# Performance work log

Hardware: AMD Instinct MI355X
Metric: run time of the kernel (lower is better)

Reference implementation:

```python
import jax, jax.numpy as jnp
import numpy as np

K = 20
EPS_BN = 1e-5

def knn_idx(x, k):
    # x: [B,N,C] -> k nearest neighbor indices [B,N,k] (self included, as in DGCNN)
    sq = jnp.sum(x * x, axis=-1)                       # [B,N]
    inner = jnp.einsum('bnc,bmc->bnm', x, x)           # [B,N,N]
    neg_dist = 2.0 * inner - sq[:, :, None] - sq[:, None, :]
    _, idx = jax.lax.top_k(neg_dist, k)
    return jax.lax.stop_gradient(idx)

def edge_feat(x, idx):
    # x: [B,N,C], idx: [B,N,k] -> [B,N,k,2C] = cat([x_j - x_i, x_i])
    nbr = jax.vmap(lambda xb, ib: xb[ib])(x, idx)      # [B,N,k,C]
    ctr = jnp.broadcast_to(x[:, :, None, :], nbr.shape)
    return jnp.concatenate([nbr - ctr, ctr], axis=-1)

def edge_conv(x, W, g, b, k):
    e = edge_feat(x, knn_idx(x, k))                    # dynamic kNN graph per layer
    h = jnp.einsum('bnkc,cd->bnkd', e, W)              # 1x1 conv2d
    h = h * (g / jnp.sqrt(1.0 + EPS_BN)) + b           # BN eval (mean=0, var=1)
    return jnp.max(jax.nn.leaky_relu(h, 0.2), axis=2)  # max over neighbors -> [B,N,d]

def layer_norm(x, g, b):
    m = jnp.mean(x, axis=-1, keepdims=True)
    v = jnp.var(x, axis=-1, keepdims=True)
    return (x - m) * jax.lax.rsqrt(v + 1e-5) * g + b

def setup_inputs():
    key = jax.random.key(0)
    B, N = 2, 4096
    ks = jax.random.split(key, 16)
    w = lambda i, shape: jax.random.normal(ks[i], shape, jnp.float32) * 0.05
    ones = lambda d: jnp.ones((d,), jnp.float32)
    zeros = lambda d: jnp.zeros((d,), jnp.float32)
    return dict(
        xyz=jax.random.normal(ks[0], (N, 3), jnp.float32),
        scale=jax.random.normal(ks[1], (N, 3), jnp.float32),
        rot=jax.random.normal(ks[2], (N, 4), jnp.float32),
        opacity=jax.random.normal(ks[3], (N, 1), jnp.float32),
        color=jax.random.normal(ks[4], (N, 3), jnp.float32),
        pose=jax.random.normal(ks[5], (B, 75), jnp.float32),
        lbs_weights=jax.random.normal(ks[6], (N, 24), jnp.float32),
        Wc1=w(7, (226, 64)), g1=ones(64), b1=zeros(64),
        Wc2=w(8, (128, 64)), g2=ones(64), b2=zeros(64),
        Wc3=w(9, (128, 128)), g3=ones(128), b3=zeros(128),
        Wc4=w(10, (256, 256)), g4=ones(256), b4=zeros(256),
        Wc5=w(11, (512, 128)), g5=ones(128), b5=zeros(128),
        Wo1=w(12, (128, 128)), bo1=zeros(128), lg1=ones(128), lb1=zeros(128),
        Wo2=w(13, (128, 128)), bo2=zeros(128), lg2=ones(128), lb2=zeros(128),
        Wo3=w(14, (128, 38)), bo3=zeros(38),
    )

def reference(xyz, scale, rot, opacity, color, pose, lbs_weights,
              Wc1, g1, b1, Wc2, g2, b2, Wc3, g3, b3, Wc4, g4, b4, Wc5, g5, b5,
              Wo1, bo1, lg1, lb1, Wo2, bo2, lg2, lb2, Wo3, bo3):
    B, N = pose.shape[0], xyz.shape[0]
    gfeat = jnp.concatenate([xyz, scale, rot, opacity, color], axis=-1)   # [N,14]
    feats = jnp.concatenate([
        jnp.broadcast_to(gfeat[None], (B, N, gfeat.shape[-1])),
        jnp.broadcast_to(lbs_weights[None], (B, N, lbs_weights.shape[-1])),
        jnp.broadcast_to(pose[:, None, :], (B, N, pose.shape[-1])),
    ], axis=-1)                                                            # [B,N,113]
    # DGCNN graph encoder (dynamic kNN EdgeConv stack)
    x1 = edge_conv(feats, Wc1, g1, b1, K)   # [B,N,64]
    x2 = edge_conv(x1, Wc2, g2, b2, K)      # [B,N,64]
    x3 = edge_conv(x2, Wc3, g3, b3, K)      # [B,N,128]
    x4 = edge_conv(x3, Wc4, g4, b4, K)      # [B,N,256]
    cat = jnp.concatenate([x1, x2, x3, x4], axis=-1)                      # [B,N,512]
    gf = jax.nn.leaky_relu(
        jnp.einsum('bnc,cd->bnd', cat, Wc5) * (g5 / jnp.sqrt(1.0 + EPS_BN)) + b5, 0.2)
    # offset predictor MLP
    h = jax.nn.leaky_relu(layer_norm(gf @ Wo1 + bo1, lg1, lb1), 0.2)
    h = jax.nn.leaky_relu(layer_norm(h @ Wo2 + bo2, lg2, lb2), 0.2)
    off = h @ Wo3 + bo3                                                   # [B,N,38]
    # residual add of gaussian offsets (first 14 dims), lbs offsets raw (last 24)
    out = jnp.concatenate([gfeat[None] + off[..., :14], off[..., 14:]], axis=-1)
    return out                                                            # [B,N,38]
```

## Files before the change

### kernel.cpp

```cpp
#include <hip/hip_runtime.h>
#include <math.h>

#define KNN 20
#define BN_INV 0.9999950000374997f

__device__ __forceinline__ unsigned f2o(float f){
    unsigned u = __float_as_uint(f);
    return (u >> 31) ? ~u : (u | 0x80000000u);
}
__device__ __forceinline__ float o2f(unsigned u){
    return __uint_as_float((u >> 31) ? (u & 0x7fffffffu) : ~u);
}
__device__ __forceinline__ float leaky(float v){ return v > 0.f ? v : 0.2f * v; }

__global__ __launch_bounds__(128) void build_feats_kernel(
    const float* __restrict__ xyz, const float* __restrict__ scale,
    const float* __restrict__ rot, const float* __restrict__ opac,
    const float* __restrict__ color, const float* __restrict__ pose,
    const float* __restrict__ lbs, float* __restrict__ feats,
    float* __restrict__ sqout, int N)
{
    __shared__ float sred[2];
    int row = blockIdx.x;
    int b = row / N, n = row % N;
    int c = threadIdx.x;
    float v = 0.f;
    if      (c <   3) v = xyz  [n*3 + c];
    else if (c <   6) v = scale[n*3 + c-3];
    else if (c <  10) v = rot  [n*4 + c-6];
    else if (c <  11) v = opac [n];
    else if (c <  14) v = color[n*3 + c-11];
    else if (c <  38) v = lbs  [n*24 + c-14];
    else if (c < 113) v = pose [b*75 + c-38];
    if (c < 116) feats[(long)row*116 + c] = v;
    float ss = v * v;
    #pragma unroll
    for (int off = 32; off; off >>= 1) ss += __shfl_xor(ss, off);
    if ((c & 63) == 0) sred[c >> 6] = ss;
    __syncthreads();
    if (c == 0) sqout[row] = sred[0] + sred[1];
}


template<int C>
__global__ __launch_bounds__(256) void dist_gemm_kernel(
    const float* __restrict__ x, int N, int CP, float* __restrict__ G)
{
    __shared__ __align__(16) float smem[9216];
    float (*xi)[36] = (float(*)[36])smem;
    float (*xj)[36] = (float(*)[36])(smem + 128*36);

    const int q = blockIdx.x;
    int bjt = (int)((sqrtf(8.f*(float)q + 1.f) - 1.f) * 0.5f);
    while ((bjt+1)*(bjt+2)/2 <= q) ++bjt;
    while (bjt*(bjt+1)/2 > q) --bjt;
    const int bit = q - bjt*(bjt+1)/2;
    const int bi = bit * 128;
    const int bj = bjt * 128;

    const int b  = blockIdx.z;
    const int t  = threadIdx.x;
    const int tx = t & 15, ty = t >> 4;
    const int CP4 = CP / 4;
    const long base = (long)b * N;
    const float4* xp = (const float4*)x;

    float acc[8][8] = {};

    for (int c0 = 0; c0 < C; c0 += 32){
        const int KC  = (C - c0 < 32) ? (C - c0) : 32;
        const int KC4 = KC >> 2;
        __syncthreads();
        if (KC4 == 8){
            for (int f = t; f < 128 * 8; f += 256){
                int r = f >> 3, c4 = f & 7;
                *(float4*)&xi[r][c4 * 4] = xp[(base + bi + r) * CP4 + (c0 >> 2) + c4];
                *(float4*)&xj[r][c4 * 4] = xp[(base + bj + r) * CP4 + (c0 >> 2) + c4];
            }
        } else {
            for (int f = t; f < 128 * KC4; f += 256){
                int r = f / KC4, c4 = f - r * KC4;
                *(float4*)&xi[r][c4 * 4] = xp[(base + bi + r) * CP4 + (c0 >> 2) + c4];
                *(float4*)&xj[r][c4 * 4] = xp[(base + bj + r) * CP4 + (c0 >> 2) + c4];
            }
        }
        __syncthreads();
        for (int c = 0; c < KC; c += 4){
            float4 A[8], Bv[8];
            #pragma unroll
            for (int ii = 0; ii < 8; ++ii) A[ii]  = *(const float4*)&xi[ty + 16*ii][c];
            #pragma unroll
            for (int jj = 0; jj < 8; ++jj) Bv[jj] = *(const float4*)&xj[tx + 16*jj][c];
            #pragma unroll
            for (int ii = 0; ii < 8; ++ii)
                #pragma unroll
                for (int jj = 0; jj < 8; ++jj){
                    acc[ii][jj] = fmaf(A[ii].x, Bv[jj].x, acc[ii][jj]);
                    acc[ii][jj] = fmaf(A[ii].y, Bv[jj].y, acc[ii][jj]);
                    acc[ii][jj] = fmaf(A[ii].z, Bv[jj].z, acc[ii][jj]);
                    acc[ii][jj] = fmaf(A[ii].w, Bv[jj].w, acc[ii][jj]);
                }
        }
    }

    #pragma unroll
    for (int ii = 0; ii < 8; ++ii){
        long rbase = (base + bi + ty + 16*ii) * N + bj;
        #pragma unroll
        for (int jj = 0; jj < 8; ++jj)
            G[rbase + tx + 16*jj] = acc[ii][jj];
    }

    if (bi != bj){
        float (*tr)[132] = (float(*)[132])smem;
        #pragma unroll
        for (int h = 0; h < 2; ++h){
            __syncthreads();
            #pragma unroll
            for (int ii = 0; ii < 8; ++ii)
                #pragma unroll
                for (int jj = 4*h; jj < 4*h + 4; ++jj)
                    tr[tx + 16*(jj - 4*h)][ty + 16*ii] = acc[ii][jj];
            __syncthreads();
            const int cc = (t & 31) * 4;
            const int r0 = t >> 5;
            #pragma unroll
            for (int f = 0; f < 8; ++f){
                int r = r0 + 8 * f;
                *(float4*)&G[(base + bj + 64*h + r) * N + bi + cc] = *(const float4*)&tr[r][cc];
            }
        }
    }
}

#define TCAP 256
__global__ __launch_bounds__(256) void topk_kernel(
    const float* __restrict__ G, const float* __restrict__ sq,
    int N, int* __restrict__ idx_out)
{
    __shared__ unsigned smax[256];
    __shared__ unsigned cand_u[TCAP];
    __shared__ int      cand_j[TCAP];
    __shared__ unsigned cand_cnt;
    __shared__ unsigned sTu;

    const int row = blockIdx.x;
    const int b   = row >> 12;
    const int t   = threadIdx.x;
    const float4* g4  = (const float4*)(G  + (long)row * 4096);
    const float4* sq4 = (const float4*)(sq + (long)b   * 4096);

    unsigned u[16];
    #pragma unroll
    for (int qq = 0; qq < 4; ++qq){
        int v4 = t + 256 * qq;
        float4 gg = g4[v4];
        float4 ss = sq4[v4];
        u[4*qq+0] = f2o(fmaf(2.f, gg.x, -ss.x));
        u[4*qq+1] = f2o(fmaf(2.f, gg.y, -ss.y));
        u[4*qq+2] = f2o(fmaf(2.f, gg.z, -ss.z));
        u[4*qq+3] = f2o(fmaf(2.f, gg.w, -ss.w));
    }

    unsigned mu = u[0];
    #pragma unroll
    for (int q = 1; q < 16; ++q) mu = u[q] > mu ? u[q] : mu;
    smax[t] = mu;
    if (t == 0) cand_cnt = 0;
    __syncthreads();

    int rank = 0;
    for (int k = 0; k < 256; ++k){
        unsigned ou = smax[k];
        rank += (ou > mu) || (ou == mu && k < t);
    }
    if (rank == KNN - 1) sTu = mu;
    __syncthreads();
    const unsigned Tu = sTu;

    #pragma unroll
    for (int qq = 0; qq < 4; ++qq)
        #pragma unroll
        for (int m = 0; m < 4; ++m){
            int q = 4*qq + m;
            if (u[q] >= Tu){
                unsigned p = atomicAdd(&cand_cnt, 1u);
                if (p < TCAP){ cand_u[p] = u[q]; cand_j[p] = 4*(t + 256*qq) + m; }
            }
        }
    __syncthreads();
    const int cc = (int)cand_cnt;

    if (cc <= TCAP){
        if (t < cc){
            unsigned cu = cand_u[t]; int cj = cand_j[t];
            int r = 0;
            for (int k = 0; k < cc; ++k){
                unsigned ou = cand_u[k];
                r += (ou > cu) || (ou == cu && cand_j[k] < cj);
            }
            if (r < KNN) idx_out[(long)row * KNN + r] = cj;
        }
    } else {
        __shared__ unsigned rv[4]; __shared__ int ri[4]; __shared__ int gj_;
        unsigned lv = 0u; int lj = 0x7fffffff;
        #pragma unroll
        for (int q = 0; q < 16; ++q)
            if (u[q] > lv){ lv = u[q]; lj = 4*(t + 256*(q>>2)) + (q&3); }
        for (int it = 0; it < KNN; ++it){
            unsigned bv = lv; int bj = lj;
            #pragma unroll
            for (int off = 32; off; off >>= 1){
                unsigned ov = __shfl_xor(bv, off);
                int      oj = __shfl_xor(bj, off);
                if (ov > bv || (ov == bv && oj < bj)){ bv = ov; bj = oj; }
            }
            if ((t & 63) == 0){ rv[t >> 6] = bv; ri[t >> 6] = bj; }
            __syncthreads();
            if (t == 0){
                unsigned fv = rv[0]; int fj = ri[0];
                #pragma unroll
                for (int w = 1; w < 4; ++w)
                    if (rv[w] > fv || (rv[w] == fv && ri[w] < fj)){ fv = rv[w]; fj = ri[w]; }
                gj_ = fj;
                idx_out[(long)row * KNN + it] = fj;
            }
            __syncthreads();
            int fj = gj_;
            if (fj >= 0 && ((fj >> 2) & 255) == t){
                u[((fj >> 10) << 2) | (fj & 3)] = 0u;
                lv = 0u; lj = 0x7fffffff;
                #pragma unroll
                for (int q = 0; q < 16; ++q)
                    if (u[q] > lv){ lv = u[q]; lj = 4*(t + 256*(q>>2)) + (q&3); }
            }
            __syncthreads();
        }
    }
}


__device__ __forceinline__ void wcat_emit(const float* __restrict__ W, int C, int D,
                                          int i, float* __restrict__ dst)
{
    int TWOD = 2 * D;
    int c = i / TWOD, n = i - c * TWOD;
    float v = 0.f;
    if (c < C) v = (n < D) ? W[c*D + n] : (W[(C + c)*D + (n - D)] - W[c*D + (n - D)]);
    dst[i] = v;
}

__global__ void prep_all_wcat_kernel(
    const float* __restrict__ Wc1, const float* __restrict__ Wc2,
    const float* __restrict__ Wc3, const float* __restrict__ Wc4,
    float* __restrict__ Wcat)
{
    int i = blockIdx.x * 256 + threadIdx.x;
    if      (i <  14848) wcat_emit(Wc1, 113,  64, i,          Wcat);
    else if (i <  23040) wcat_emit(Wc2,  64,  64, i - 14848,  Wcat + 14848);
    else if (i <  39424) wcat_emit(Wc3,  64, 128, i - 23040,  Wcat + 23040);
    else if (i < 104960) wcat_emit(Wc4, 128, 256, i - 39424,  Wcat + 39424);
}

__global__ __launch_bounds__(256) void gemm_pq_kernel(
    const float* __restrict__ X, int CP, const float* __restrict__ Wcat,
    const float* __restrict__ g, const float* __restrict__ bias,
    int D, int TWOD, float* __restrict__ PQ)
{
    __shared__ __align__(16) float As[128][36];
    __shared__ __align__(16) float Bs[32][132];
    const int bi = blockIdx.x * 128;
    const int bn = blockIdx.y * 128;
    const int t  = threadIdx.x;
    const int tx = t & 15, ty = t >> 4;
    const int CP4 = CP / 4;
    const float4* xp = (const float4*)X;

    float acc[8][8] = {};
    float4 pa[4], pb[4];

    int c0 = 0;
    int KC4 = ((CP < 32) ? CP : 32) >> 2;
    #pragma unroll
    for (int s = 0; s < 4; ++s){
        int f = t + 256*s;
        if (f < 128*KC4){
            int r = f / KC4, c4 = f - r*KC4;
            pa[s] = xp[(long)(bi + r)*CP4 + c4];
        }
        if (f < 128*KC4){
            int r = f >> 5, c4 = f & 31;
            pb[s] = *(const float4*)&Wcat[(long)r * TWOD + bn + c4*4];
        }
    }

    for (;;){
        __syncthreads();
        #pragma unroll
        for (int s = 0; s < 4; ++s){
            int f = t + 256*s;
            if (f < 128*KC4){
                int r = f / KC4, c4 = f - r*KC4;
                *(float4*)&As[r][c4*4] = pa[s];
            }
            if (f < 128*KC4){
                int r = f >> 5, c4 = f & 31;
                *(float4*)&Bs[r][c4*4] = pb[s];
            }
        }
        __syncthreads();
        const int KC  = KC4 * 4;
        const int c0n = c0 + 32;
        int KC4n = 0;
        if (c0n < CP){
            KC4n = (((CP - c0n) < 32) ? (CP - c0n) : 32) >> 2;
            #pragma unroll
            for (int s = 0; s < 4; ++s){
                int f = t + 256*s;
                if (f < 128*KC4n){
                    int r = f / KC4n, c4 = f - r*KC4n;
                    pa[s] = xp[(long)(bi + r)*CP4 + (c0n >> 2) + c4];
                }
                if (f < 128*KC4n){
                    int r = f >> 5, c4 = f & 31;
                    pb[s] = *(const float4*)&Wcat[(long)(c0n + r) * TWOD + bn + c4*4];
                }
            }
        }
        for (int c = 0; c < KC; c += 4){
            float4 A[8];
            #pragma unroll
            for (int ii = 0; ii < 8; ++ii) A[ii] = *(const float4*)&As[ty + 16*ii][c];
            float Bv0[8], Bv1[8], Bv2[8], Bv3[8];
            #pragma unroll
            for (int jj = 0; jj < 8; ++jj){
                Bv0[jj] = Bs[c+0][tx + 16*jj];
                Bv1[jj] = Bs[c+1][tx + 16*jj];
                Bv2[jj] = Bs[c+2][tx + 16*jj];
                Bv3[jj] = Bs[c+3][tx + 16*jj];
            }
            #pragma unroll
            for (int ii = 0; ii < 8; ++ii)
                #pragma unroll
                for (int jj = 0; jj < 8; ++jj){
                    acc[ii][jj] = fmaf(A[ii].x, Bv0[jj], acc[ii][jj]);
                    acc[ii][jj] = fmaf(A[ii].y, Bv1[jj], acc[ii][jj]);
                    acc[ii][jj] = fmaf(A[ii].z, Bv2[jj], acc[ii][jj]);
                    acc[ii][jj] = fmaf(A[ii].w, Bv3[jj], acc[ii][jj]);
                }
        }
        if (c0n >= CP) break;
        c0 = c0n; KC4 = KC4n;
    }

    #pragma unroll
    for (int jj = 0; jj < 8; ++jj){
        int n = bn + tx + 16*jj;
        int d = (n < D) ? n : n - D;
        float gg = g[d] * BN_INV;
        float bb = (n < D) ? 0.f : bias[d];
        #pragma unroll
        for (int ii = 0; ii < 8; ++ii)
            PQ[(long)(bi + ty + 16*ii) * TWOD + n] = fmaf(acc[ii][jj], gg, bb);
    }
}

__global__ __launch_bounds__(256) void gemm_pq64_kernel(
    const float* __restrict__ X, int CP, const float* __restrict__ Wcat,
    const float* __restrict__ g, const float* __restrict__ bias,
    int D, int TWOD, float* __restrict__ PQ)
{
    __shared__ __align__(16) float As[64][36];
    __shared__ __align__(16) float Bs[32][68];
    const int bi = blockIdx.x * 64;
    const int bn = blockIdx.y * 64;
    const int t  = threadIdx.x;
    const int tx = t & 15, ty = t >> 4;
    const int CP4 = CP / 4;
    const float4* xp = (const float4*)X;

    float acc[4][4] = {};
    float4 pa[2], pb[2];

    int c0 = 0;
    int KC4 = ((CP < 32) ? CP : 32) >> 2;
    #pragma unroll
    for (int s = 0; s < 2; ++s){
        int f = t + 256*s;
        if (f < 64*KC4){
            int r = f / KC4, c4 = f - r*KC4;
            pa[s] = xp[(long)(bi + r)*CP4 + c4];
        }
        if (f < 64*KC4){
            int r = f >> 4, c4 = f & 15;
            pb[s] = *(const float4*)&Wcat[(long)r * TWOD + bn + c4*4];
        }
    }

    for (;;){
        __syncthreads();
        #pragma unroll
        for (int s = 0; s < 2; ++s){
            int f = t + 256*s;
            if (f < 64*KC4){
                int r = f / KC4, c4 = f - r*KC4;
                *(float4*)&As[r][c4*4] = pa[s];
            }
            if (f < 64*KC4){
                int r = f >> 4, c4 = f & 15;
                *(float4*)&Bs[r][c4*4] = pb[s];
            }
        }
        __syncthreads();
        const int KC  = KC4 * 4;
        const int c0n = c0 + 32;
        int KC4n = 0;
        if (c0n < CP){
            KC4n = (((CP - c0n) < 32) ? (CP - c0n) : 32) >> 2;
            #pragma unroll
            for (int s = 0; s < 2; ++s){
                int f = t + 256*s;
                if (f < 64*KC4n){
                    int r = f / KC4n, c4 = f - r*KC4n;
                    pa[s] = xp[(long)(bi + r)*CP4 + (c0n >> 2) + c4];
                }
                if (f < 64*KC4n){
                    int r = f >> 4, c4 = f & 15;
                    pb[s] = *(const float4*)&Wcat[(long)(c0n + r) * TWOD + bn + c4*4];
                }
            }
        }
        for (int c = 0; c < KC; c += 4){
            float4 A[4];
            #pragma unroll
            for (int ii = 0; ii < 4; ++ii) A[ii] = *(const float4*)&As[ty + 16*ii][c];
            float B0[4], B1[4], B2[4], B3[4];
            #pragma unroll
            for (int jj = 0; jj < 4; ++jj){
                B0[jj] = Bs[c+0][tx + 16*jj];
                B1[jj] = Bs[c+1][tx + 16*jj];
                B2[jj] = Bs[c+2][tx + 16*jj];
                B3[jj] = Bs[c+3][tx + 16*jj];
            }
            #pragma unroll
            for (int ii = 0; ii < 4; ++ii)
                #pragma unroll
                for (int jj = 0; jj < 4; ++jj){
                    acc[ii][jj] = fmaf(A[ii].x, B0[jj], acc[ii][jj]);
                    acc[ii][jj] = fmaf(A[ii].y, B1[jj], acc[ii][jj]);
                    acc[ii][jj] = fmaf(A[ii].z, B2[jj], acc[ii][jj]);
                    acc[ii][jj] = fmaf(A[ii].w, B3[jj], acc[ii][jj]);
                }
        }
        if (c0n >= CP) break;
        c0 = c0n; KC4 = KC4n;
    }

    #pragma unroll
    for (int jj = 0; jj < 4; ++jj){
        int n = bn + tx + 16*jj;
        int d = (n < D) ? n : n - D;
        float gg = g[d] * BN_INV;
        float bb = (n < D) ? 0.f : bias[d];
        #pragma unroll
        for (int ii = 0; ii < 4; ++ii)
            PQ[(long)(bi + ty + 16*ii) * TWOD + n] = fmaf(acc[ii][jj], gg, bb);
    }
}

template<int D, int RPB>
__global__ __launch_bounds__(256) void gather_max_kernel(
    const float* __restrict__ PQ, const int* __restrict__ idx, int N,
    float* __restrict__ y, float* __restrict__ sqout)
{
    __shared__ int   lidx[RPB][KNN];
    __shared__ float sred[4];
    const int rb = blockIdx.x * RPB;
    const int t  = threadIdx.x;
    if (t < RPB * KNN) lidx[t / KNN][t % KNN] = idx[(long)rb * KNN + t];
    __syncthreads();

    const int r = t / D, d = t - r * D;
    const int row = rb + r;
    const long base = (long)(row / N) * N;
    const int TWOD = 2 * D;

    float q = PQ[(long)row * TWOD + D + d];
    float m = -INFINITY;
    #pragma unroll
    for (int k = 0; k < KNN; ++k){
        int j = lidx[r][k];
        m = fmaxf(m, PQ[(base + j) * TWOD + d]);
    }
    float val = leaky(m + q);
    y[(long)row * D + d] = val;

    float ss = val * val;
    #pragma unroll
    for (int off = 32; off; off >>= 1) ss += __shfl_xor(ss, off);
    if ((t & 63) == 0) sred[t >> 6] = ss;
    __syncthreads();
    if (d == 0){
        constexpr int WPR = D / 64;
        float s = 0.f;
        int w0 = (r * D) >> 6;
        #pragma unroll
        for (int w = 0; w < WPR; ++w) s += sred[w0 + w];
        sqout[row] = s;
    }
}


__global__ __launch_bounds__(256) void head_gemm1_kernel(
    const float* __restrict__ x1, const float* __restrict__ x2,
    const float* __restrict__ x3, const float* __restrict__ x4,
    const float* __restrict__ Wc5, const float* __restrict__ g5,
    const float* __restrict__ b5, float* __restrict__ gf, int R)
{
    __shared__ __align__(16) float As[64][68];
    __shared__ __align__(16) float Bs[64][68];
    const int bi = blockIdx.x * 64;
    const int bn = blockIdx.y * 64;
    const int t  = threadIdx.x;
    const int tx = t & 15, ty = t >> 4;

    float acc[4][4] = {};

    #pragma unroll 1
    for (int kc = 0; kc < 8; ++kc){
        const float* src; int ld, coff;
        if      (kc == 0){ src = x1; ld = 64;  coff = 0; }
        else if (kc == 1){ src = x2; ld = 64;  coff = 0; }
        else if (kc <  4){ src = x3; ld = 128; coff = (kc-2)*64; }
        else             { src = x4; ld = 256; coff = (kc-4)*64; }
        __syncthreads();
        for (int f = t; f < 64*16; f += 256){
            int r = f >> 4, c4 = f & 15;
            *(float4*)&As[r][c4*4] = *(const float4*)&src[(long)(bi + r)*ld + coff + c4*4];
            *(float4*)&Bs[r][c4*4] = *(const float4*)&Wc5[(long)(kc*64 + r)*128 + bn + c4*4];
        }
        __syncthreads();
        for (int c = 0; c < 64; c += 4){
            float4 A[4];
            #pragma unroll
            for (int ii = 0; ii < 4; ++ii) A[ii] = *(const float4*)&As[ty + 16*ii][c];
            float B0[4], B1[4], B2[4], B3[4];
            #pragma unroll
            for (int jj = 0; jj < 4; ++jj){
                B0[jj] = Bs[c+0][tx + 16*jj];
                B1[jj] = Bs[c+1][tx + 16*jj];
                B2[jj] = Bs[c+2][tx + 16*jj];
                B3[jj] = Bs[c+3][tx + 16*jj];
            }
            #pragma unroll
            for (int ii = 0; ii < 4; ++ii)
                #pragma unroll
                for (int jj = 0; jj < 4; ++jj){
                    acc[ii][jj] = fmaf(A[ii].x, B0[jj], acc[ii][jj]);
                    acc[ii][jj] = fmaf(A[ii].y, B1[jj], acc[ii][jj]);
                    acc[ii][jj] = fmaf(A[ii].z, B2[jj], acc[ii][jj]);
                    acc[ii][jj] = fmaf(A[ii].w, B3[jj], acc[ii][jj]);
                }
        }
    }

    #pragma unroll
    for (int jj = 0; jj < 4; ++jj){
        int n = bn + tx + 16*jj;
        float gg = g5[n] * BN_INV, bb = b5[n];
        #pragma unroll
        for (int ii = 0; ii < 4; ++ii)
            gf[(long)(bi + ty + 16*ii)*128 + n] = leaky(fmaf(acc[ii][jj], gg, bb));
    }
}

__global__ __launch_bounds__(256) void head_lngemm_kernel(
    const float* __restrict__ hin, const float* __restrict__ W,
    const float* __restrict__ bo, const float* __restrict__ lg,
    const float* __restrict__ lb, float* __restrict__ hout, int R)
{
    __shared__ __align__(16) float As[64][68];
    __shared__ __align__(16) float Bs[64][132];
    const int bi = blockIdx.x * 64;
    const int t  = threadIdx.x;
    const int tx = t & 15, ty = t >> 4;

    float acc[4][8] = {};

    #pragma unroll 1
    for (int kc = 0; kc < 2; ++kc){
        __syncthreads();
        for (int f = t; f < 64*16; f += 256){
            int r = f >> 4, c4 = f & 15;
            *(float4*)&As[r][c4*4] = *(const float4*)&hin[(long)(bi + r)*128 + kc*64 + c4*4];
        }
        for (int f = t; f < 64*32; f += 256){
            int r = f >> 5, c4 = f & 31;
            *(float4*)&Bs[r][c4*4] = *(const float4*)&W[(long)(kc*64 + r)*128 + c4*4];
        }
        __syncthreads();
        for (int c = 0; c < 64; c += 4){
            float4 A[4];
            #pragma unroll
            for (int ii = 0; ii < 4; ++ii) A[ii] = *(const float4*)&As[ty + 16*ii][c];
            float B0[8], B1[8], B2[8], B3[8];
            #pragma unroll
            for (int jj = 0; jj < 8; ++jj){
                B0[jj] = Bs[c+0][tx + 16*jj];
                B1[jj] = Bs[c+1][tx + 16*jj];
                B2[jj] = Bs[c+2][tx + 16*jj];
                B3[jj] = Bs[c+3][tx + 16*jj];
            }
            #pragma unroll
            for (int ii = 0; ii < 4; ++ii)
                #pragma unroll
                for (int jj = 0; jj < 8; ++jj){
                    acc[ii][jj] = fmaf(A[ii].x, B0[jj], acc[ii][jj]);
                    acc[ii][jj] = fmaf(A[ii].y, B1[jj], acc[ii][jj]);
                    acc[ii][jj] = fmaf(A[ii].z, B2[jj], acc[ii][jj]);
                    acc[ii][jj] = fmaf(A[ii].w, B3[jj], acc[ii][jj]);
                }
        }
    }

    float bon[8], lgn[8], lbn[8];
    #pragma unroll
    for (int jj = 0; jj < 8; ++jj){
        int n = tx + 16*jj;
        bon[jj] = bo[n]; lgn[jj] = lg[n]; lbn[jj] = lb[n];
    }
    #pragma unroll
    for (int ii = 0; ii < 4; ++ii){
        float s1 = 0.f, s2 = 0.f;
        #pragma unroll
        for (int jj = 0; jj < 8; ++jj){
            float a = acc[ii][jj] + bon[jj];
            acc[ii][jj] = a;
            s1 += a; s2 += a*a;
        }
        #pragma unroll
        for (int off = 8; off; off >>= 1){
            s1 += __shfl_xor(s1, off);
            s2 += __shfl_xor(s2, off);
        }
        float m = s1 * (1.f/128.f);
        float v = s2 * (1.f/128.f) - m*m;
        float rinv = rsqrtf(v + 1e-5f);
        long r = bi + ty + 16*ii;
        #pragma unroll
        for (int jj = 0; jj < 8; ++jj)
            hout[r*128 + tx + 16*jj] = leaky((acc[ii][jj] - m) * rinv * lgn[jj] + lbn[jj]);
    }
}

#define OP 16
__global__ __launch_bounds__(256) void head_out_kernel(
    const float* __restrict__ h, const float* __restrict__ feats,
    const float* __restrict__ Wo3, const float* __restrict__ bo3,
    float* __restrict__ out, int R)
{
    __shared__ __align__(16) float hs[OP][132];
    __shared__ float f14[OP][14];
    const int t  = threadIdx.x;
    const long p0 = (long)blockIdx.x * OP;

    for (int f = t; f < OP*32; f += 256){
        int r = f >> 5, c4 = f & 31;
        *(float4*)&hs[r][c4*4] = *(const float4*)&h[(p0 + r)*128 + c4*4];
    }
    if (t < OP*14) f14[t/14][t%14] = feats[(p0 + t/14)*116 + t%14];
    __syncthreads();

    const int w = t >> 6, l = t & 63;
    if (l < 38){
        float o[4];
        float bt = bo3[l];
        #pragma unroll
        for (int pp = 0; pp < 4; ++pp) o[pp] = bt;
        for (int c = 0; c < 128; ++c){
            float wv = Wo3[c*38 + l];
            #pragma unroll
            for (int pp = 0; pp < 4; ++pp)
                o[pp] = fmaf(hs[w*4 + pp][c], wv, o[pp]);
        }
        #pragma unroll
        for (int pp = 0; pp < 4; ++pp){
            int p = w*4 + pp;
            float val = o[pp] + ((l < 14) ? f14[p][l] : 0.f);
            out[(p0 + p)*38 + l] = val;
        }
    }
}

__global__ __launch_bounds__(256) void knn_kernel(
    const float* __restrict__ x, int N, int CP4, int* __restrict__ idx_out)
{
    __shared__ float4 xi4[32];
    __shared__ float drow[4096];
    __shared__ float rv[4];
    __shared__ int   ri[4];

    int row = blockIdx.x;
    int b = row / N;
    int t = threadIdx.x;
    const float4* xp = (const float4*)x;

    if (t < CP4) xi4[t] = xp[(long)row * CP4 + t];
    __syncthreads();

    long bb = (long)b * N * CP4;
    for (int j = t; j < N; j += 256){
        const float4* p = xp + bb + (long)j * CP4;
        float acc = 0.f;
        #pragma unroll 4
        for (int c = 0; c < CP4; ++c){
            float4 xv = p[c], yv = xi4[c];
            float dx = xv.x - yv.x, dy = xv.y - yv.y;
            float dz = xv.z - yv.z, dw = xv.w - yv.w;
            acc += dx*dx + dy*dy + dz*dz + dw*dw;
        }
        drow[j] = -acc;
    }
    __syncthreads();

    for (int it = 0; it < KNN; ++it){
        float bv = -INFINITY; int bi = N;
        for (int j = t; j < N; j += 256){
            float v = drow[j];
            if (v > bv){ bv = v; bi = j; }
        }
        #pragma unroll
        for (int off = 32; off > 0; off >>= 1){
            float ov = __shfl_xor(bv, off);
            int   oi = __shfl_xor(bi, off);
            if (ov > bv || (ov == bv && oi < bi)){ bv = ov; bi = oi; }
        }
        if ((t & 63) == 0){ rv[t >> 6] = bv; ri[t >> 6] = bi; }
        __syncthreads();
        if (t == 0){
            float fv = rv[0]; int fi = ri[0];
            #pragma unroll
            for (int w = 1; w < 4; ++w){
                if (rv[w] > fv || (rv[w] == fv && ri[w] < fi)){ fv = rv[w]; fi = ri[w]; }
            }
            idx_out[(long)row * KNN + it] = fi;
            drow[fi] = -INFINITY;
        }
        __syncthreads();
    }
}

template<int D, int KPT>
__global__ __launch_bounds__(256) void edge_conv_kernel(
    const float* __restrict__ x, int N, int C, int CP,
    const float* __restrict__ W, const float* __restrict__ g,
    const float* __restrict__ bias, const int* __restrict__ idx,
    float* __restrict__ y, float* __restrict__ sqout)
{
    __shared__ float xi[128];
    __shared__ float nbr[KNN * 128];
    __shared__ float t2[D];
    __shared__ unsigned um[D];
    __shared__ float sred[4];

    int row = blockIdx.x;
    int b = row / N;
    int t = threadIdx.x;

    for (int c = t; c < C; c += 256) xi[c] = x[(long)row * CP + c];
    for (int kk = 0; kk < KNN; ++kk){
        int j = idx[(long)row * KNN + kk];
        long nb = ((long)b * N + j) * CP;
        for (int c = t; c < C; c += 256) nbr[kk * C + c] = x[nb + c];
    }
    __syncthreads();

    for (int d = t; d < D; d += 256){
        float s = 0.f;
        for (int c = 0; c < C; ++c) s += xi[c] * W[(C + c) * D + d];
        t2[d] = s; um[d] = 0u;
    }
    __syncthreads();

    const int d  = t % D;
    const int kg = t / D;
    float s[KPT];
    #pragma unroll
    for (int q = 0; q < KPT; ++q) s[q] = t2[d];

    const float* nb0 = &nbr[(kg * KPT) * C];
    for (int c = 0; c < C; ++c){
        float w   = W[c * D + d];
        float xic = xi[c];
        #pragma unroll
        for (int q = 0; q < KPT; ++q)
            s[q] += (nb0[q * C + c] - xic) * w;
    }
    float g_ = g[d] * BN_INV, b_ = bias[d];
    float m = -INFINITY;
    #pragma unroll
    for (int q = 0; q < KPT; ++q)
        m = fmaxf(m, leaky(s[q] * g_ + b_));
    atomicMax(&um[d], f2o(m));
    __syncthreads();

    float ss = 0.f;
    for (int dd = t; dd < D; dd += 256){
        float val = o2f(um[dd]);
        y[(long)row * D + dd] = val;
        ss += val * val;
    }
    #pragma unroll
    for (int off = 32; off; off >>= 1) ss += __shfl_xor(ss, off);
    if ((t & 63) == 0) sred[t >> 6] = ss;
    __syncthreads();
    if (t == 0) sqout[row] = sred[0] + sred[1] + sred[2] + sred[3];
}

#define HP 8
__global__ __launch_bounds__(128) void head_kernel(
    const float* __restrict__ x1, const float* __restrict__ x2,
    const float* __restrict__ x3, const float* __restrict__ x4,
    const float* __restrict__ feats,
    const float* __restrict__ Wc5, const float* __restrict__ g5, const float* __restrict__ b5,
    const float* __restrict__ Wo1, const float* __restrict__ bo1,
    const float* __restrict__ lg1, const float* __restrict__ lb1,
    const float* __restrict__ Wo2, const float* __restrict__ bo2,
    const float* __restrict__ lg2, const float* __restrict__ lb2,
    const float* __restrict__ Wo3, const float* __restrict__ bo3,
    float* __restrict__ out, int N, int R)
{
    __shared__ __align__(16) float cat[HP][520];
    __shared__ __align__(16) float hb[HP][132];
    __shared__ float wsum[2][HP], wsq[2][HP];
    __shared__ float f14[HP][14];

    const int t = threadIdx.x;
    const long p0 = (long)blockIdx.x * HP;
    const int wid = t >> 6;

    long rows[HP];
    #pragma unroll
    for (int p = 0; p < HP; ++p){
        long row = p0 + p; if (row >= R) row = R - 1;
        rows[p] = row;
        cat[p][t]       = (t < 64) ? x1[row*64 + t] : x2[row*64 + (t-64)];
        cat[p][128 + t] = x3[row*128 + t];
        cat[p][256 + t] = x4[row*256 + t];
        cat[p][384 + t] = x4[row*256 + 128 + t];
        if (t < 14) f14[p][t] = feats[row*116 + t];
    }
    __syncthreads();

    const float g5t = g5[t] * BN_INV, b5t = b5[t];
    float acc[HP];
    #pragma unroll
    for (int p = 0; p < HP; ++p) acc[p] = 0.f;
    for (int c4 = 0; c4 < 128; ++c4){
        float w0 = Wc5[(4*c4+0)*128 + t];
        float w1 = Wc5[(4*c4+1)*128 + t];
        float w2 = Wc5[(4*c4+2)*128 + t];
        float w3 = Wc5[(4*c4+3)*128 + t];
        #pragma unroll
        for (int p = 0; p < HP; ++p){
            float4 cv = *(const float4*)&cat[p][4*c4];
            acc[p] = fmaf(cv.x, w0, acc[p]);
            acc[p] = fmaf(cv.y, w1, acc[p]);
            acc[p] = fmaf(cv.z, w2, acc[p]);
            acc[p] = fmaf(cv.w, w3, acc[p]);
        }
    }
    #pragma unroll
    for (int p = 0; p < HP; ++p) hb[p][t] = leaky(fmaf(acc[p], g5t, b5t));
    __syncthreads();

    for (int layer = 0; layer < 2; ++layer){
        const float* W  = layer ? Wo2 : Wo1;
        const float* bo = layer ? bo2 : bo1;
        const float* lg = layer ? lg2 : lg1;
        const float* lb = layer ? lb2 : lb1;
        float a2[HP];
        float bot = bo[t];
        #pragma unroll
        for (int p = 0; p < HP; ++p) a2[p] = bot;
        for (int c4 = 0; c4 < 32; ++c4){
            float w0 = W[(4*c4+0)*128 + t];
            float w1 = W[(4*c4+1)*128 + t];
            float w2 = W[(4*c4+2)*128 + t];
            float w3 = W[(4*c4+3)*128 + t];
            #pragma unroll
            for (int p = 0; p < HP; ++p){
                float4 hv = *(const float4*)&hb[p][4*c4];
                a2[p] = fmaf(hv.x, w0, a2[p]);
                a2[p] = fmaf(hv.y, w1, a2[p]);
                a2[p] = fmaf(hv.z, w2, a2[p]);
                a2[p] = fmaf(hv.w, w3, a2[p]);
            }
        }
        #pragma unroll
        for (int p = 0; p < HP; ++p){
            float s1 = a2[p], s2 = a2[p]*a2[p];
            #pragma unroll
            for (int off = 32; off; off >>= 1){
                s1 += __shfl_xor(s1, off);
                s2 += __shfl_xor(s2, off);
            }
            if ((t & 63) == 0){ wsum[wid][p] = s1; wsq[wid][p] = s2; }
        }
        __syncthreads();
        float lgt = lg[t], lbt = lb[t];
        float hn[HP];
        #pragma unroll
        for (int p = 0; p < HP; ++p){
            float m  = (wsum[0][p] + wsum[1][p]) * (1.f/128.f);
            float v  = (wsq[0][p]  + wsq[1][p])  * (1.f/128.f) - m*m;
            float dm = a2[p] - m;
            hn[p] = leaky(dm * rsqrtf(v + 1e-5f) * lgt + lbt);
        }
        __syncthreads();
        #pragma unroll
        for (int p = 0; p < HP; ++p) hb[p][t] = hn[p];
        __syncthreads();
    }

    if (t < 38){
        float o[HP];
        float bt = bo3[t];
        #pragma unroll
        for (int p = 0; p < HP; ++p) o[p] = bt;
        for (int c = 0; c < 128; ++c){
            float w = Wo3[c*38 + t];
            #pragma unroll
            for (int p = 0; p < HP; ++p) o[p] = fmaf(hb[p][c], w, o[p]);
        }
        #pragma unroll
        for (int p = 0; p < HP; ++p){
            float val = o[p] + ((t < 14) ? f14[p][t] : 0.f);
            out[rows[p]*38 + t] = val;
        }
    }
}

extern "C" void kernel_launch(void* const* d_in, const int* in_sizes, int n_in,
                              void* d_out, int out_size, void* d_ws, size_t ws_size,
                              hipStream_t stream)
{
    const float* xyz  = (const float*)d_in[0];
    const float* scal = (const float*)d_in[1];
    const float* rot  = (const float*)d_in[2];
    const float* opac = (const float*)d_in[3];
    const float* colr = (const float*)d_in[4];
    const float* pose = (const float*)d_in[5];
    const float* lbs  = (const float*)d_in[6];
    const float* Wc1 = (const float*)d_in[7];  const float* g1 = (const float*)d_in[8];  const float* b1 = (const float*)d_in[9];
    const float* Wc2 = (const float*)d_in[10]; const float* g2 = (const float*)d_in[11]; const float* b2 = (const float*)d_in[12];
    const float* Wc3 = (const float*)d_in[13]; const float* g3 = (const float*)d_in[14]; const float* b3 = (const float*)d_in[15];
    const float* Wc4 = (const float*)d_in[16]; const float* g4 = (const float*)d_in[17]; const float* b4 = (const float*)d_in[18];
    const float* Wc5 = (const float*)d_in[19]; const float* g5 = (const float*)d_in[20]; const float* b5 = (const float*)d_in[21];
    const float* Wo1 = (const float*)d_in[22]; const float* bo1 = (const float*)d_in[23];
    const float* lg1 = (const float*)d_in[24]; const float* lb1 = (const float*)d_in[25];
    const float* Wo2 = (const float*)d_in[26]; const float* bo2 = (const float*)d_in[27];
    const float* lg2 = (const float*)d_in[28]; const float* lb2 = (const float*)d_in[29];
    const float* Wo3 = (const float*)d_in[30]; const float* bo3 = (const float*)d_in[31];

    const int N = in_sizes[0] / 3;
    const int B = in_sizes[5] / 75;
    const int R = B * N;

    char* ws = (char*)d_ws;
    size_t o = 0;
    float* feats = (float*)(ws + o); o += (size_t)R * 116 * 4;
    float* x1    = (float*)(ws + o); o += (size_t)R * 64  * 4;
    float* x2    = (float*)(ws + o); o += (size_t)R * 64  * 4;
    float* x3    = (float*)(ws + o); o += (size_t)R * 128 * 4;
    float* x4    = (float*)(ws + o); o += (size_t)R * 256 * 4;
    int*   idx   = (int*)  (ws + o); o += (size_t)R * KNN * 4;
    float* sq    = (float*)(ws + o); o += (size_t)R * 4;
    float* Wcat  = (float*)(ws + o); o += (size_t)104960 * 4;
    float* G     = (float*)(ws + o);
    float* PQ    = G;
    float* gf    = G;
    float* h1    = G + (size_t)R * 128;
    float* h2    = G + (size_t)R * 256;
    size_t need  = o + (size_t)B * N * N * 4;

    const bool fast = (N == 4096) && (ws_size >= need);

    build_feats_kernel<<<R, 128, 0, stream>>>(xyz, scal, rot, opac, colr, pose, lbs, feats, sq, N);

    if (fast){
        const int NT = 32;
        dim3 gg(NT*(NT+1)/2, 1, B);
        float* Wcat1 = Wcat;
        float* Wcat2 = Wcat + 14848;
        float* Wcat3 = Wcat + 23040;
        float* Wcat4 = Wcat + 39424;

        prep_all_wcat_kernel<<<(104960 + 255)/256, 256, 0, stream>>>(Wc1, Wc2, Wc3, Wc4, Wcat);

        dist_gemm_kernel<116><<<gg, 256, 0, stream>>>(feats, N, 116, G);
        topk_kernel<<<R, 256, 0, stream>>>(G, sq, N, idx);
        gemm_pq64_kernel<<<dim3(R/64, 2), 256, 0, stream>>>(feats, 116, Wcat1, g1, b1, 64, 128, PQ);
        gather_max_kernel<64, 4><<<R/4, 256, 0, stream>>>(PQ, idx, N, x1, sq);

        dist_gemm_kernel<64><<<gg, 256, 0, stream>>>(x1, N, 64, G);
        topk_kernel<<<R, 256, 0, stream>>>(G, sq, N, idx);
        gemm_pq64_kernel<<<dim3(R/64, 2), 256, 0, stream>>>(x1, 64, Wcat2, g2, b2, 64, 128, PQ);
        gather_max_kernel<64, 4><<<R/4, 256, 0, stream>>>(PQ, idx, N, x2, sq);

        dist_gemm_kernel<64><<<gg, 256, 0, stream>>>(x2, N, 64, G);
        topk_kernel<<<R, 256, 0, stream>>>(G, sq, N, idx);
        gemm_pq64_kernel<<<dim3(R/64, 4), 256, 0, stream>>>(x2, 64, Wcat3, g3, b3, 128, 256, PQ);
        gather_max_kernel<128, 2><<<R/2, 256, 0, stream>>>(PQ, idx, N, x3, sq);

        dist_gemm_kernel<128><<<gg, 256, 0, stream>>>(x3, N, 128, G);
        topk_kernel<<<R, 256, 0, stream>>>(G, sq, N, idx);
        gemm_pq_kernel<<<dim3(R/128, 4), 256, 0, stream>>>(x3, 128, Wcat4, g4, b4, 256, 512, PQ);
        gather_max_kernel<256, 1><<<R, 256, 0, stream>>>(PQ, idx, N, x4, sq);

        head_gemm1_kernel<<<dim3(R/64, 2), 256, 0, stream>>>(x1, x2, x3, x4, Wc5, g5, b5, gf, R);
        head_lngemm_kernel<<<R/64, 256, 0, stream>>>(gf, Wo1, bo1, lg1, lb1, h1, R);
        head_lngemm_kernel<<<R/64, 256, 0, stream>>>(h1, Wo2, bo2, lg2, lb2, h2, R);
        head_out_kernel<<<R/OP, 256, 0, stream>>>(h2, feats, Wo3, bo3, (float*)d_out, R);
    } else {
        knn_kernel<<<R, 256, 0, stream>>>(feats, N, 116/4, idx);
        edge_conv_kernel<64, 5><<<R, 256, 0, stream>>>(feats, N, 113, 116, Wc1, g1, b1, idx, x1, sq);
        knn_kernel<<<R, 256, 0, stream>>>(x1, N, 64/4, idx);
        edge_conv_kernel<64, 5><<<R, 256, 0, stream>>>(x1, N, 64, 64, Wc2, g2, b2, idx, x2, sq);
        knn_kernel<<<R, 256, 0, stream>>>(x2, N, 64/4, idx);
        edge_conv_kernel<128, 10><<<R, 256, 0, stream>>>(x2, N, 64, 64, Wc3, g3, b3, idx, x3, sq);
        knn_kernel<<<R, 256, 0, stream>>>(x3, N, 128/4, idx);
        edge_conv_kernel<256, 20><<<R, 256, 0, stream>>>(x3, N, 128, 128, Wc4, g4, b4, idx, x4, sq);

        head_kernel<<<(R + HP - 1)/HP, 128, 0, stream>>>(x1, x2, x3, x4, feats,
                                           Wc5, g5, b5, Wo1, bo1, lg1, lb1,
                                           Wo2, bo2, lg2, lb2, Wo3, bo3,
                                           (float*)d_out, N, R);
    }
}
```

Before: 810.6 us.

## Process kNN distance GEMM and top-k per batch to shrink the Gram buffer

The distance GEMM and top-k kernels now run once per batch element from a host loop instead of once over the whole batch via the grid z dimension. The Gram matrix buffer shrinks from B*N*N to N*N floats (64MB for N=4096), which may fit better in the large last-level cache between the GEMM write and the top-k read. In exchange there are twice as many launches and each GEMM grid is half as large, which lowers parallelism per launch.

New measurement: 923.3 us. 13.9% more time.

```diff
diff --git a/kernel.cpp b/kernel.cpp
--- a/kernel.cpp
+++ b/kernel.cpp
@@ -58,11 +58,9 @@
     const int bi = bit * 128;
     const int bj = bjt * 128;
 
-    const int b  = blockIdx.z;
     const int t  = threadIdx.x;
     const int tx = t & 15, ty = t >> 4;
     const int CP4 = CP / 4;
-    const long base = (long)b * N;
     const float4* xp = (const float4*)x;
 
     float acc[8][8] = {};
@@ -74,14 +72,14 @@
         if (KC4 == 8){
             for (int f = t; f < 128 * 8; f += 256){
                 int r = f >> 3, c4 = f & 7;
-                *(float4*)&xi[r][c4 * 4] = xp[(base + bi + r) * CP4 + (c0 >> 2) + c4];
-                *(float4*)&xj[r][c4 * 4] = xp[(base + bj + r) * CP4 + (c0 >> 2) + c4];
+                *(float4*)&xi[r][c4 * 4] = xp[(long)(bi + r) * CP4 + (c0 >> 2) + c4];
+                *(float4*)&xj[r][c4 * 4] = xp[(long)(bj + r) * CP4 + (c0 >> 2) + c4];
             }
         } else {
             for (int f = t; f < 128 * KC4; f += 256){
                 int r = f / KC4, c4 = f - r * KC4;
-                *(float4*)&xi[r][c4 * 4] = xp[(base + bi + r) * CP4 + (c0 >> 2) + c4];
-                *(float4*)&xj[r][c4 * 4] = xp[(base + bj + r) * CP4 + (c0 >> 2) + c4];
+                *(float4*)&xi[r][c4 * 4] = xp[(long)(bi + r) * CP4 + (c0 >> 2) + c4];
+                *(float4*)&xj[r][c4 * 4] = xp[(long)(bj + r) * CP4 + (c0 >> 2) + c4];
             }
         }
         __syncthreads();
@@ -105,7 +103,7 @@
 
     #pragma unroll
     for (int ii = 0; ii < 8; ++ii){
-        long rbase = (base + bi + ty + 16*ii) * N + bj;
+        long rbase = (long)(bi + ty + 16*ii) * N + bj;
         #pragma unroll
         for (int jj = 0; jj < 8; ++jj)
             G[rbase + tx + 16*jj] = acc[ii][jj];
@@ -127,7 +125,7 @@
             #pragma unroll
             for (int f = 0; f < 8; ++f){
                 int r = r0 + 8 * f;
-                *(float4*)&G[(base + bj + 64*h + r) * N + bi + cc] = *(const float4*)&tr[r][cc];
+                *(float4*)&G[(long)(bj + 64*h + r) * N + bi + cc] = *(const float4*)&tr[r][cc];
             }
         }
     }
@@ -145,10 +143,9 @@
     __shared__ unsigned sTu;
 
     const int row = blockIdx.x;
-    const int b   = row >> 12;
     const int t   = threadIdx.x;
-    const float4* g4  = (const float4*)(G  + (long)row * 4096);
-    const float4* sq4 = (const float4*)(sq + (long)b   * 4096);
+    const float4* g4  = (const float4*)(G + (long)row * 4096);
+    const float4* sq4 = (const float4*)sq;
 
     unsigned u[16];
     #pragma unroll
@@ -982,7 +979,7 @@
     float* gf    = G;
     float* h1    = G + (size_t)R * 128;
     float* h2    = G + (size_t)R * 256;
-    size_t need  = o + (size_t)B * N * N * 4;
+    size_t need  = o + (size_t)N * N * 4;
 
     const bool fast = (N == 4096) && (ws_size >= need);
 
@@ -990,7 +987,7 @@
 
     if (fast){
         const int NT = 32;
-        dim3 gg(NT*(NT+1)/2, 1, B);
+        dim3 gg(NT*(NT+1)/2, 1, 1);
         float* Wcat1 = Wcat;
         float* Wcat2 = Wcat + 14848;
         float* Wcat3 = Wcat + 23040;
@@ -998,23 +995,31 @@
 
         prep_all_wcat_kernel<<<(104960 + 255)/256, 256, 0, stream>>>(Wc1, Wc2, Wc3, Wc4, Wcat);
 
-        dist_gemm_kernel<116><<<gg, 256, 0, stream>>>(feats, N, 116, G);
-        topk_kernel<<<R, 256, 0, stream>>>(G, sq, N, idx);
+        for (int b = 0; b < B; ++b){
+            dist_gemm_kernel<116><<<gg, 256, 0, stream>>>(feats + (size_t)b*N*116, N, 116, G);
+            topk_kernel<<<N, 256, 0, stream>>>(G, sq + (size_t)b*N, N, idx + (size_t)b*N*KNN);
+        }
         gemm_pq64_kernel<<<dim3(R/64, 2), 256, 0, stream>>>(feats, 116, Wcat1, g1, b1, 64, 128, PQ);
         gather_max_kernel<64, 4><<<R/4, 256, 0, stream>>>(PQ, idx, N, x1, sq);
 
-        dist_gemm_kernel<64><<<gg, 256, 0, stream>>>(x1, N, 64, G);
-        topk_kernel<<<R, 256, 0, stream>>>(G, sq, N, idx);
+        for (int b = 0; b < B; ++b){
+            dist_gemm_kernel<64><<<gg, 256, 0, stream>>>(x1 + (size_t)b*N*64, N, 64, G);
+            topk_kernel<<<N, 256, 0, stream>>>(G, sq + (size_t)b*N, N, idx + (size_t)b*N*KNN);
+        }
         gemm_pq64_kernel<<<dim3(R/64, 2), 256, 0, stream>>>(x1, 64, Wcat2, g2, b2, 64, 128, PQ);
         gather_max_kernel<64, 4><<<R/4, 256, 0, stream>>>(PQ, idx, N, x2, sq);
 
-        dist_gemm_kernel<64><<<gg, 256, 0, stream>>>(x2, N, 64, G);
-        topk_kernel<<<R, 256, 0, stream>>>(G, sq, N, idx);
+        for (int b = 0; b < B; ++b){
+            dist_gemm_kernel<64><<<gg, 256, 0, stream>>>(x2 + (size_t)b*N*64, N, 64, G);
+            topk_kernel<<<N, 256, 0, stream>>>(G, sq + (size_t)b*N, N, idx + (size_t)b*N*KNN);
+        }
         gemm_pq64_kernel<<<dim3(R/64, 4), 256, 0, stream>>>(x2, 64, Wcat3, g3, b3, 128, 256, PQ);
         gather_max_kernel<128, 2><<<R/2, 256, 0, stream>>>(PQ, idx, N, x3, sq);
 
-        dist_gemm_kernel<128><<<gg, 256, 0, stream>>>(x3, N, 128, G);
-        topk_kernel<<<R, 256, 0, stream>>>(G, sq, N, idx);
+        for (int b = 0; b < B; ++b){
+            dist_gemm_kernel<128><<<gg, 256, 0, stream>>>(x3 + (size_t)b*N*128, N, 128, G);
+            topk_kernel<<<N, 256, 0, stream>>>(G, sq + (size_t)b*N, N, idx + (size_t)b*N*KNN);
+        }
         gemm_pq_kernel<<<dim3(R/128, 4), 256, 0, stream>>>(x3, 128, Wcat4, g4, b4, 256, 512, PQ);
         gather_max_kernel<256, 1><<<R, 256, 0, stream>>>(PQ, idx, N, x4, sq);
 
```
